# Kernel tuning notes

Measured on AMD Instinct MI355X. Metric: run time of the kernel, lower is better.

The kernel has to match this reference:

```python
import jax, jax.numpy as jnp
import numpy as np

GAIN = 1.0
EPS = 1e-08


def setup_inputs() -> dict:
    key = jax.random.key(0)
    k1, k2, k3 = jax.random.split(key, 3)
    B, H, W, Cin, Cout, K = 8, 64, 64, 512, 512, 3
    x = jax.random.normal(k1, (B, H, W, Cin), dtype=jnp.float32)
    style = jax.random.normal(k2, (B, Cin), dtype=jnp.float32)
    kernel = jax.random.normal(k3, (K, K, Cin, Cout), dtype=jnp.float32)
    return {"x": x, "style": style, "kernel": kernel}


def reference(x, style, kernel):
    # x: [B,H,W,Cin], style: [B,Cin], kernel: [K,K,Cin,Cout]
    B, H, W, Cin = x.shape
    K = kernel.shape[0]
    Cout = kernel.shape[-1]
    scale = GAIN / np.sqrt(K * K * Cin)

    # modulate: per-sample weights [B,K,K,Cin,Cout]
    ww = (scale * kernel)[None] * style[:, None, None, :, None]
    # demodulate
    sigma = jax.lax.rsqrt(jnp.sum(jnp.square(ww), axis=(1, 2, 3)) + EPS)  # [B,Cout]
    ww = ww * sigma[:, None, None, None, :]

    # grouped conv via batch->channel reshape (groups = B)
    x_nchw = jnp.transpose(x, (0, 3, 1, 2)).reshape(1, B * Cin, H, W)
    # weights to HWIO with per-sample groups stacked on output channels
    w = jnp.transpose(ww, (1, 2, 3, 0, 4)).reshape(K, K, Cin, B * Cout)
    out = jax.lax.conv_general_dilated(
        x_nchw, w,
        window_strides=(1, 1),
        padding='SAME',
        dimension_numbers=('NCHW', 'HWIO', 'NCHW'),
        feature_group_count=B,
    )  # [1, B*Cout, H, W]
    out = out.reshape(B, Cout, H, W)
    return jnp.transpose(out, (0, 2, 3, 1))  # [B,H,W,Cout]
```

## Files before the change

kernel.cpp:

```cpp
#include <hip/hip_runtime.h>

typedef __bf16 bf16x8 __attribute__((ext_vector_type(8)));
typedef float f32x4 __attribute__((ext_vector_type(4)));

#define SCALE_F 0.014731391274719738f
#define SCALE2_F 2.170138888888889e-4f

__device__ __forceinline__ ushort f2bf(float f) {
    uint x = __float_as_uint(f);
    uint r = (x + 0x7fffu + ((x >> 16) & 1u)) >> 16;
    return (ushort)r;
}

__device__ __forceinline__ void async_cp16(const void* g, void* l) {
    __builtin_amdgcn_global_load_lds(
        (const __attribute__((address_space(1))) void*)g,
        (__attribute__((address_space(3))) void*)l, 16, 0, 0);
}


__global__ void k_prep(const float* __restrict__ kern, float* __restrict__ Q,
                       const float* __restrict__ x, ushort* __restrict__ xp) {
    int bx = blockIdx.x;
    if (bx < 1024) {
        int idx = bx * 256 + threadIdx.x;
        float s = 0.f;
#pragma unroll
        for (int t = 0; t < 9; ++t) { float v = kern[t * 262144 + idx]; s += v * v; }
        Q[idx] = s * SCALE2_F;
        return;
    }
    int idx = (bx - 1024) * 256 + threadIdx.x;
    int pos = idx >> 6, e = idx & 63;
    int b = pos / 4356, rem = pos - b * 4356;
    int hp = rem / 66, wp = rem - hp * 66;
    int ci0 = e << 3;
    uint4 o = make_uint4(0u, 0u, 0u, 0u);
    if (hp >= 1 && hp <= 64 && wp >= 1 && wp <= 64) {
        const float4* s =
            (const float4*)(x + (((size_t)(b * 4096 + (hp - 1) * 64 + (wp - 1))) << 9) + ci0);
        float4 v0 = s[0], v1 = s[1];
        o.x = (uint)f2bf(v0.x) | ((uint)f2bf(v0.y) << 16);
        o.y = (uint)f2bf(v0.z) | ((uint)f2bf(v0.w) << 16);
        o.z = (uint)f2bf(v1.x) | ((uint)f2bf(v1.y) << 16);
        o.w = (uint)f2bf(v1.z) | ((uint)f2bf(v1.w) << 16);
    }
    *(uint4*)(xp + (((size_t)pos) << 9) + ci0) = o;
}

__global__ void k_sigma(const float* __restrict__ style, const float* __restrict__ Q,
                        float* __restrict__ sig) {
    __shared__ float s2[512];
    int b = blockIdx.x, cq = blockIdx.y;
    int t = threadIdx.x;
    {
        float s0 = style[b * 512 + t];
        float s1 = style[b * 512 + 256 + t];
        s2[t] = s0 * s0;
        s2[256 + t] = s1 * s1;
    }
    __syncthreads();
    int co = cq * 64 + (t & 63);
    int ciq = (t >> 6) * 128;
    float acc = 0.f;
#pragma unroll 16
    for (int ci = 0; ci < 128; ++ci) acc += s2[ciq + ci] * Q[(ciq + ci) * 512 + co];
    __shared__ float part[4][64];
    part[t >> 6][t & 63] = acc;
    __syncthreads();
    if (t < 64) {
        float v = part[0][t] + part[1][t] + part[2][t] + part[3][t];
        sig[b * 512 + cq * 64 + t] = rsqrtf(v + 1e-8f);
    }
}

__global__ void k_wt(const float* __restrict__ kern, const float* __restrict__ style,
                     const float* __restrict__ sig, ushort* __restrict__ wT) {
    __shared__ float tile[64][65];
    int tap = blockIdx.y;
    int ci0 = (blockIdx.x >> 3) << 6, co0 = (blockIdx.x & 7) << 6;
    int t = threadIdx.x;
    int col = t & 63, rq = t >> 6;
#pragma unroll
    for (int r = 0; r < 16; ++r) {
        int ci_l = r * 4 + rq;
        tile[ci_l][col] = SCALE_F * kern[(size_t)(tap * 512 + ci0 + ci_l) * 512 + co0 + col];
    }
    __syncthreads();
#pragma unroll 1
    for (int b = 0; b < 8; ++b) {
#pragma unroll
        for (int r = 0; r < 4; ++r) {
            int q = r * 256 + t;
            int co_l = q >> 4;
            int ciq = (q & 15) << 2;
            float sg = sig[b * 512 + co0 + co_l];
            float v0 = tile[ciq + 0][co_l] * style[b * 512 + ci0 + ciq + 0] * sg;
            float v1 = tile[ciq + 1][co_l] * style[b * 512 + ci0 + ciq + 1] * sg;
            float v2 = tile[ciq + 2][co_l] * style[b * 512 + ci0 + ciq + 2] * sg;
            float v3 = tile[ciq + 3][co_l] * style[b * 512 + ci0 + ciq + 3] * sg;
            uint lo = (uint)f2bf(v0) | ((uint)f2bf(v1) << 16);
            uint hi = (uint)f2bf(v2) | ((uint)f2bf(v3) << 16);
            *(uint2*)(&wT[((size_t)(b * 9 + tap) * 512 + co0 + co_l) * 512 + ci0 + ciq]) =
                make_uint2(lo, hi);
        }
    }
}

__global__ __launch_bounds__(512, 2) void conv_mfma(const ushort* __restrict__ xpad,
                                                    const ushort* __restrict__ wT,
                                                    float* __restrict__ out) {
    extern __shared__ char lds[];

    const int wg = blockIdx.x;
    const int swz = (wg & 7) * 32 + (wg >> 3);
    const int mt = swz & 15;
    const int nt = (swz >> 4) & 1;
    const int b = swz >> 5;

    const int tid = threadIdx.x;
    const int l = tid & 63, wv = tid >> 6;
    const int wm = (wv >> 2) * 128;
    const int wn = (wv & 3) * 64;
    const int ha = wv >> 2;
    const int hb = (wv & 3) >> 1;

    const int rl = l >> 3;
    const int g = (l & 7) ^ rl;
    const ushort* baseA[2][2];
    const ushort* baseB[2][2];
#pragma unroll
    for (int h = 0; h < 2; ++h)
#pragma unroll
        for (int i = 0; i < 2; ++i) {
            int rloc = wv * 16 + i * 8 + rl;
            int R = h * 128 + rloc;
            baseA[h][i] = xpad + ((size_t)((b * 66 + mt * 4 + (R >> 6)) * 66 + (R & 63))) * 512 + g * 8;
            baseB[h][i] = wT + ((size_t)(b * 9 * 512 + nt * 256 + R)) * 512 + g * 8;
        }
    const int so0 = (wv * 16) * 128;
    const int so1 = (wv * 16 + 8) * 128;

    auto offA = [](int t) -> int {
        int tap = t >> 3;
        int ky = (tap * 11) >> 5;
        int kx = tap - ky * 3;
        return (ky * 66 + kx) * 512 + ((t & 7) << 6);
    };
    auto offB = [](int t) -> int { return (t >> 3) * 262144 + ((t & 7) << 6); };

    auto stA = [&](int t, int h) {
        int ts = t > 71 ? 71 : t;
        int o = offA(ts);
        char* d = lds + (t & 1) * 32768 + h * 16384;
        async_cp16(baseA[h][0] + o, d + so0);
        async_cp16(baseA[h][1] + o, d + so1);
    };
    auto stB = [&](int t, int h) {
        int ts = t > 71 ? 71 : t;
        int o = offB(ts);
        char* d = lds + 65536 + (t & 1) * 32768 + h * 16384;
        async_cp16(baseB[h][0] + o, d + so0);
        async_cp16(baseB[h][1] + o, d + so1);
    };

    const int frow = l & 15;
    const int fchunk_base = l >> 4;
    const int fxor = l & 7;

    f32x4 acc[8][4];
#pragma unroll
    for (int mi = 0; mi < 8; ++mi)
#pragma unroll
        for (int ni = 0; ni < 4; ++ni) acc[mi][ni] = (f32x4){0.f, 0.f, 0.f, 0.f};

    bf16x8 bq[4][2];
    bf16x8 aqE[2][2], aqO[2][2];

    auto rdB = [&](const char* bB) {
#pragma unroll
        for (int kk = 0; kk < 2; ++kk)
#pragma unroll
            for (int ni = 0; ni < 4; ++ni) {
                int r = (wn & 64) + ni * 16 + frow;
                bq[ni][kk] = *(const bf16x8*)(bB + r * 128 +
                                              (((kk * 4 + fchunk_base) ^ fxor) * 16));
            }
    };
    auto rdA = [&](bf16x8 (&aq)[2][2], const char* aB, int q) {
#pragma unroll
        for (int m2 = 0; m2 < 2; ++m2)
#pragma unroll
            for (int kk = 0; kk < 2; ++kk) {
                int r = (2 * q + m2) * 16 + frow;
                aq[m2][kk] = *(const bf16x8*)(aB + r * 128 +
                                              (((kk * 4 + fchunk_base) ^ fxor) * 16));
            }
    };

#define FENCE_L4                                                        \
    {                                                                   \
        __builtin_amdgcn_sched_barrier(0);                              \
        asm volatile("s_waitcnt lgkmcnt(4)" ::: "memory");              \
        __builtin_amdgcn_s_barrier();                                   \
        __builtin_amdgcn_sched_barrier(0);                              \
    }
#define FENCE_L12                                                       \
    {                                                                   \
        __builtin_amdgcn_sched_barrier(0);                              \
        asm volatile("s_waitcnt lgkmcnt(12)" ::: "memory");             \
        __builtin_amdgcn_s_barrier();                                   \
        __builtin_amdgcn_sched_barrier(0);                              \
    }
#define FENCE_V4L4                                                      \
    {                                                                   \
        __builtin_amdgcn_sched_barrier(0);                              \
        asm volatile("s_waitcnt vmcnt(4) lgkmcnt(4)" ::: "memory");     \
        __builtin_amdgcn_s_barrier();                                   \
        __builtin_amdgcn_sched_barrier(0);                              \
    }
#define FENCE_V2L4                                                      \
    {                                                                   \
        __builtin_amdgcn_sched_barrier(0);                              \
        asm volatile("s_waitcnt vmcnt(2) lgkmcnt(4)" ::: "memory");     \
        __builtin_amdgcn_s_barrier();                                   \
        __builtin_amdgcn_sched_barrier(0);                              \
    }

#define MFMA16(Q, AQ)                                                                  \
    do {                                                                               \
        __builtin_amdgcn_s_setprio(1);                                                 \
        _Pragma("unroll") for (int kk = 0; kk < 2; ++kk)                               \
            _Pragma("unroll") for (int ni = 0; ni < 4; ++ni)                           \
                _Pragma("unroll") for (int m2 = 0; m2 < 2; ++m2)                       \
                    acc[2 * (Q) + m2][ni] = __builtin_amdgcn_mfma_f32_16x16x32_bf16(   \
                        (AQ)[m2][kk], bq[ni][kk], acc[2 * (Q) + m2][ni], 0, 0, 0);     \
        __builtin_amdgcn_s_setprio(0);                                                 \
    } while (0)

    const char* Ab0 = lds + ha * 16384;
    const char* Ab1 = lds + 32768 + ha * 16384;
    const char* Bb0 = lds + 65536 + hb * 16384;
    const char* Bb1 = lds + 98304 + hb * 16384;

    stA(0, 0); stA(0, 1);
    stB(0, 0); stB(0, 1);
    asm volatile("s_waitcnt vmcnt(0)" ::: "memory");
    __builtin_amdgcn_sched_barrier(0);
    __builtin_amdgcn_s_barrier();
    __builtin_amdgcn_sched_barrier(0);
    stB(1, 0); stB(1, 1);
    rdA(aqE, Ab0, 0);
    rdB(Bb0);

#pragma unroll 1
    for (int i = 0; i < 36; ++i) {
        const int T = 2 * i;
        rdA(aqO, Ab0, 1); stA(T + 1, 0);
        FENCE_L12; MFMA16(0, aqE);
        rdA(aqE, Ab0, 2); stA(T + 1, 1);
        FENCE_V4L4; MFMA16(1, aqO);
        rdA(aqO, Ab0, 3); stB(T + 2, 0);
        FENCE_V2L4; MFMA16(2, aqE);
        rdA(aqE, Ab1, 0); stB(T + 2, 1);
        FENCE_L4; MFMA16(3, aqO);
        rdB(Bb1);
        rdA(aqO, Ab1, 1); stA(T + 2, 0);
        FENCE_L12; MFMA16(0, aqE);
        rdA(aqE, Ab1, 2); stA(T + 2, 1);
        FENCE_L4; MFMA16(1, aqO);
        rdA(aqO, Ab1, 3); stB(T + 3, 0);
        FENCE_V2L4; MFMA16(2, aqE);
        rdA(aqE, Ab0, 0); stB(T + 3, 1);
        FENCE_L4; MFMA16(3, aqO);
        rdB(Bb0);
    }

    asm volatile("s_waitcnt vmcnt(0) lgkmcnt(0)" ::: "memory");

#pragma unroll
    for (int mi = 0; mi < 8; ++mi) {
#pragma unroll
        for (int ni = 0; ni < 4; ++ni) {
#pragma unroll
            for (int r = 0; r < 4; ++r) {
                int m = mt * 256 + wm + mi * 16 + (l >> 4) * 4 + r;
                int co = nt * 256 + wn + ni * 16 + (l & 15);
                out[(((size_t)(b * 4096 + m)) << 9) + co] = acc[mi][ni][r];
            }
        }
    }
#undef MFMA16
#undef FENCE_L4
#undef FENCE_L12
#undef FENCE_V4L4
#undef FENCE_V2L4
}


extern "C" void kernel_launch(void* const* d_in, const int* in_sizes, int n_in,
                              void* d_out, int out_size, void* d_ws, size_t ws_size,
                              hipStream_t stream) {
    const float* x = (const float*)d_in[0];
    const float* style = (const float*)d_in[1];
    const float* kern = (const float*)d_in[2];
    float* out = (float*)d_out;

    char* ws = (char*)d_ws;
    ushort* xpad = (ushort*)ws;
    ushort* wT = (ushort*)(ws + 35684352);
    float* Q = (float*)(ws + 35684352 + 37748736);
    float* sig = (float*)(ws + 35684352 + 37748736 + 1048576);

    (void)hipFuncSetAttribute((const void*)conv_mfma,
                              hipFuncAttributeMaxDynamicSharedMemorySize, 131072);

    k_prep<<<9736, 256, 0, stream>>>(kern, Q, x, xpad);
    k_sigma<<<dim3(8, 8), 256, 0, stream>>>(style, Q, sig);
    k_wt<<<dim3(64, 9), 256, 0, stream>>>(kern, style, sig, wT);
    conv_mfma<<<256, 512, 131072, stream>>>(xpad, wT, out);
}
```

Measured before the change: 158.4 us.

## Fold style into activations and sigma into epilogue, share one weight tensor

Result: faster. 149.8 us (-5.4%).

```diff
diff --git a/kernel.cpp b/kernel.cpp
--- a/kernel.cpp
+++ b/kernel.cpp
@@ -18,34 +18,66 @@
         (__attribute__((address_space(3))) void*)l, 16, 0, 0);
 }
 
-
 __global__ void k_prep(const float* __restrict__ kern, float* __restrict__ Q,
-                       const float* __restrict__ x, ushort* __restrict__ xp) {
+                       const float* __restrict__ x, const float* __restrict__ style,
+                       ushort* __restrict__ xp, ushort* __restrict__ wTs) {
     int bx = blockIdx.x;
+    int t = threadIdx.x;
     if (bx < 1024) {
-        int idx = bx * 256 + threadIdx.x;
+        int idx = bx * 256 + t;
         float s = 0.f;
 #pragma unroll
-        for (int t = 0; t < 9; ++t) { float v = kern[t * 262144 + idx]; s += v * v; }
+        for (int tp = 0; tp < 9; ++tp) { float v = kern[tp * 262144 + idx]; s += v * v; }
         Q[idx] = s * SCALE2_F;
         return;
     }
-    int idx = (bx - 1024) * 256 + threadIdx.x;
-    int pos = idx >> 6, e = idx & 63;
-    int b = pos / 4356, rem = pos - b * 4356;
-    int hp = rem / 66, wp = rem - hp * 66;
-    int ci0 = e << 3;
-    uint4 o = make_uint4(0u, 0u, 0u, 0u);
-    if (hp >= 1 && hp <= 64 && wp >= 1 && wp <= 64) {
-        const float4* s =
-            (const float4*)(x + (((size_t)(b * 4096 + (hp - 1) * 64 + (wp - 1))) << 9) + ci0);
-        float4 v0 = s[0], v1 = s[1];
-        o.x = (uint)f2bf(v0.x) | ((uint)f2bf(v0.y) << 16);
-        o.y = (uint)f2bf(v0.z) | ((uint)f2bf(v0.w) << 16);
-        o.z = (uint)f2bf(v1.x) | ((uint)f2bf(v1.y) << 16);
-        o.w = (uint)f2bf(v1.z) | ((uint)f2bf(v1.w) << 16);
-    }
-    *(uint4*)(xp + (((size_t)pos) << 9) + ci0) = o;
+    if (bx < 9736) {
+        int idx = (bx - 1024) * 256 + t;
+        int pos = idx >> 6, e = idx & 63;
+        int b = pos / 4356, rem = pos - b * 4356;
+        int hp = rem / 66, wp = rem - hp * 66;
+        int ci0 = e << 3;
+        uint4 o = make_uint4(0u, 0u, 0u, 0u);
+        if (hp >= 1 && hp <= 64 && wp >= 1 && wp <= 64) {
+            const float4* s =
+                (const float4*)(x + (((size_t)(b * 4096 + (hp - 1) * 64 + (wp - 1))) << 9) + ci0);
+            const float4* st = (const float4*)(style + b * 512 + ci0);
+            float4 v0 = s[0], v1 = s[1];
+            float4 s0 = st[0], s1 = st[1];
+            o.x = (uint)f2bf(v0.x * s0.x) | ((uint)f2bf(v0.y * s0.y) << 16);
+            o.y = (uint)f2bf(v0.z * s0.z) | ((uint)f2bf(v0.w * s0.w) << 16);
+            o.z = (uint)f2bf(v1.x * s1.x) | ((uint)f2bf(v1.y * s1.y) << 16);
+            o.w = (uint)f2bf(v1.z * s1.z) | ((uint)f2bf(v1.w * s1.w) << 16);
+        }
+        *(uint4*)(xp + (((size_t)pos) << 9) + ci0) = o;
+        return;
+    }
+    __shared__ float tile[64][65];
+    int wbx = bx - 9736;
+    int tap = wbx >> 6;
+    int r64 = wbx & 63;
+    int ci0 = (r64 >> 3) << 6, co0 = (r64 & 7) << 6;
+    int col = t & 63, rq = t >> 6;
+#pragma unroll
+    for (int r = 0; r < 16; ++r) {
+        int ci_l = r * 4 + rq;
+        tile[ci_l][col] = SCALE_F * kern[(size_t)(tap * 512 + ci0 + ci_l) * 512 + co0 + col];
+    }
+    __syncthreads();
+#pragma unroll
+    for (int r = 0; r < 4; ++r) {
+        int q = r * 256 + t;
+        int co_l = q >> 4;
+        int ciq = (q & 15) << 2;
+        float v0 = tile[ciq + 0][co_l];
+        float v1 = tile[ciq + 1][co_l];
+        float v2 = tile[ciq + 2][co_l];
+        float v3 = tile[ciq + 3][co_l];
+        uint lo = (uint)f2bf(v0) | ((uint)f2bf(v1) << 16);
+        uint hi = (uint)f2bf(v2) | ((uint)f2bf(v3) << 16);
+        *(uint2*)(&wTs[((size_t)(tap * 512 + co0 + co_l)) * 512 + ci0 + ciq]) =
+            make_uint2(lo, hi);
+    }
 }
 
 __global__ void k_sigma(const float* __restrict__ style, const float* __restrict__ Q,
@@ -74,41 +106,9 @@
     }
 }
 
-__global__ void k_wt(const float* __restrict__ kern, const float* __restrict__ style,
-                     const float* __restrict__ sig, ushort* __restrict__ wT) {
-    __shared__ float tile[64][65];
-    int tap = blockIdx.y;
-    int ci0 = (blockIdx.x >> 3) << 6, co0 = (blockIdx.x & 7) << 6;
-    int t = threadIdx.x;
-    int col = t & 63, rq = t >> 6;
-#pragma unroll
-    for (int r = 0; r < 16; ++r) {
-        int ci_l = r * 4 + rq;
-        tile[ci_l][col] = SCALE_F * kern[(size_t)(tap * 512 + ci0 + ci_l) * 512 + co0 + col];
-    }
-    __syncthreads();
-#pragma unroll 1
-    for (int b = 0; b < 8; ++b) {
-#pragma unroll
-        for (int r = 0; r < 4; ++r) {
-            int q = r * 256 + t;
-            int co_l = q >> 4;
-            int ciq = (q & 15) << 2;
-            float sg = sig[b * 512 + co0 + co_l];
-            float v0 = tile[ciq + 0][co_l] * style[b * 512 + ci0 + ciq + 0] * sg;
-            float v1 = tile[ciq + 1][co_l] * style[b * 512 + ci0 + ciq + 1] * sg;
-            float v2 = tile[ciq + 2][co_l] * style[b * 512 + ci0 + ciq + 2] * sg;
-            float v3 = tile[ciq + 3][co_l] * style[b * 512 + ci0 + ciq + 3] * sg;
-            uint lo = (uint)f2bf(v0) | ((uint)f2bf(v1) << 16);
-            uint hi = (uint)f2bf(v2) | ((uint)f2bf(v3) << 16);
-            *(uint2*)(&wT[((size_t)(b * 9 + tap) * 512 + co0 + co_l) * 512 + ci0 + ciq]) =
-                make_uint2(lo, hi);
-        }
-    }
-}
-
 __global__ __launch_bounds__(512, 2) void conv_mfma(const ushort* __restrict__ xpad,
-                                                    const ushort* __restrict__ wT,
+                                                    const ushort* __restrict__ wTs,
+                                                    const float* __restrict__ sig,
                                                     float* __restrict__ out) {
     extern __shared__ char lds[];
 
@@ -136,7 +136,7 @@
             int rloc = wv * 16 + i * 8 + rl;
             int R = h * 128 + rloc;
             baseA[h][i] = xpad + ((size_t)((b * 66 + mt * 4 + (R >> 6)) * 66 + (R & 63))) * 512 + g * 8;
-            baseB[h][i] = wT + ((size_t)(b * 9 * 512 + nt * 256 + R)) * 512 + g * 8;
+            baseB[h][i] = wTs + ((size_t)(nt * 256 + R)) * 512 + g * 8;
         }
     const int so0 = (wv * 16) * 128;
     const int so1 = (wv * 16 + 8) * 128;
@@ -278,6 +278,10 @@
 
     asm volatile("s_waitcnt vmcnt(0) lgkmcnt(0)" ::: "memory");
 
+    float sg[4];
+#pragma unroll
+    for (int ni = 0; ni < 4; ++ni)
+        sg[ni] = sig[b * 512 + nt * 256 + wn + ni * 16 + (l & 15)];
 #pragma unroll
     for (int mi = 0; mi < 8; ++mi) {
 #pragma unroll
@@ -286,7 +290,7 @@
             for (int r = 0; r < 4; ++r) {
                 int m = mt * 256 + wm + mi * 16 + (l >> 4) * 4 + r;
                 int co = nt * 256 + wn + ni * 16 + (l & 15);
-                out[(((size_t)(b * 4096 + m)) << 9) + co] = acc[mi][ni][r];
+                out[(((size_t)(b * 4096 + m)) << 9) + co] = acc[mi][ni][r] * sg[ni];
             }
         }
     }
@@ -308,15 +312,14 @@
 
     char* ws = (char*)d_ws;
     ushort* xpad = (ushort*)ws;
-    ushort* wT = (ushort*)(ws + 35684352);
-    float* Q = (float*)(ws + 35684352 + 37748736);
-    float* sig = (float*)(ws + 35684352 + 37748736 + 1048576);
+    ushort* wTs = (ushort*)(ws + 35684352);
+    float* Q = (float*)(ws + 35684352 + 4718592);
+    float* sig = (float*)(ws + 35684352 + 4718592 + 1048576);
 
     (void)hipFuncSetAttribute((const void*)conv_mfma,
                               hipFuncAttributeMaxDynamicSharedMemorySize, 131072);
 
-    k_prep<<<9736, 256, 0, stream>>>(kern, Q, x, xpad);
+    k_prep<<<10312, 256, 0, stream>>>(kern, Q, x, style, xpad, wTs);
     k_sigma<<<dim3(8, 8), 256, 0, stream>>>(style, Q, sig);
-    k_wt<<<dim3(64, 9), 256, 0, stream>>>(kern, style, sig, wT);
-    conv_mfma<<<256, 512, 131072, stream>>>(xpad, wT, out);
-}
+    conv_mfma<<<256, 512, 131072, stream>>>(xpad, wTs, sig, out);
+}
```
